# Optimization experiments

Measured on AMD Instinct MI355X. Metric: run time of the kernel, lower is better.

The kernel has to match this reference:

```python
import jax, jax.numpy as jnp
import numpy as np

B, NBANDS, NCHAN, NTIME = 32, 9, 64, 4096
M = 32
C = M * NBANDS          # 288 spectral-spatial channels
SF = 4                  # strideFactor
TLEN = 2 * SF - 1       # 7 overlapping temporal windows
E = 2                   # embed_dim
H = 2                   # num_heads (head_dim = 1)
NCLASS = 4
BN_EPS = 1e-5


def _renorm(w, maxnorm):
    # torch.renorm(p=2, dim=0): clamp L2 norm of each dim-0 slice to maxnorm
    norms = jnp.sqrt(jnp.sum(w.reshape(w.shape[0], -1) ** 2, axis=1))
    scale = jnp.minimum(1.0, maxnorm / jnp.maximum(norms, 1e-7))
    return w * scale.reshape((-1,) + (1,) * (w.ndim - 1))


def _pos_embed():
    # get_1d_sincos_pos_embed_from_grid(embed_dim=2, len=7)
    pos = np.arange(TLEN, dtype=np.float32)
    omega = 1.0 / (10000.0 ** (np.arange(E // 2, dtype=np.float32) / (E / 2.0)))
    out = pos[:, None] * omega[None, :]
    return jnp.asarray(np.concatenate([np.sin(out), np.cos(out)], axis=1), jnp.float32)  # [TLEN, E]


def setup_inputs() -> dict:
    key = jax.random.key(0)
    ks = jax.random.split(key, 10)
    s = 0.1
    return {
        "x": jax.random.uniform(ks[0], (B, NBANDS, NCHAN, NTIME), jnp.float32),
        "conv_w": jax.random.normal(ks[1], (C, 1, NCHAN, 1), jnp.float32) * s,
        "conv_b": jax.random.normal(ks[2], (C,), jnp.float32) * s,
        "bn_gamma": jnp.ones((C,), jnp.float32),
        "bn_beta": jnp.zeros((C,), jnp.float32),
        "bn_mean": jnp.zeros((C,), jnp.float32),
        "bn_var": jnp.ones((C,), jnp.float32),
        "in_proj_w": jax.random.normal(ks[3], (C, 3 * E, E), jnp.float32) * s,
        "in_proj_b": jax.random.normal(ks[4], (C, 3 * E), jnp.float32) * s,
        "out_proj_w": jax.random.normal(ks[5], (C, E, E), jnp.float32) * s,
        "out_proj_b": jax.random.normal(ks[6], (C, E), jnp.float32) * s,
        "last_w": jax.random.normal(ks[7], (NCLASS, C * TLEN * E), jnp.float32) * s,
        "last_b": jax.random.normal(ks[8], (NCLASS,), jnp.float32) * s,
    }


def _forward(x, conv_w, conv_b, bn_gamma, bn_beta, bn_mean, bn_var,
             in_proj_w, in_proj_b, out_proj_w, out_proj_b, last_w, last_b):
    # --- SCB: grouped conv (nChan,1) + BatchNorm(eval) + swish ---
    w = _renorm(conv_w, 2.0)
    y = jax.lax.conv_general_dilated(
        x, w, window_strides=(1, 1), padding='VALID',
        dimension_numbers=('NCHW', 'OIHW', 'NCHW'),
        feature_group_count=NBANDS) + conv_b[None, :, None, None]      # [B,C,1,NTIME]
    y = (y - bn_mean[None, :, None, None]) * jax.lax.rsqrt(bn_var + BN_EPS)[None, :, None, None]
    y = y * bn_gamma[None, :, None, None] + bn_beta[None, :, None, None]
    y = y * jax.nn.sigmoid(y)  # swish

    # --- overlapping temporal windows stacked on dim 2 ---
    ts = NTIME // (SF * 2)
    xs = jnp.concatenate([y[:, :, :, i * ts:(i + 2) * ts] for i in range(TLEN)], axis=2)  # [B,C,TLEN,2ts]

    # --- tempo_layer: log-var, RMS/mean shape factor ---
    var = jnp.log(jnp.clip(jnp.var(xs, axis=3, keepdims=True, ddof=1), 1e-6, 1e6))
    mean_ = jnp.mean(xs, axis=3, keepdims=True)
    x_rms = jnp.sqrt(jnp.mean(xs ** 2, axis=3, keepdims=True))
    feat = jnp.concatenate([var, x_rms / mean_], axis=3)               # [B,C,TLEN,E]

    # --- batched per-channel multihead self-attention (replaces C-way loop) ---
    yq = feat + _pos_embed()[None, None]                               # [B,C,T,E]
    qkv = jnp.einsum('bcte,cfe->bctf', yq, in_proj_w) + in_proj_b[None, :, None, :]
    q, k, v = jnp.split(qkv, 3, axis=3)
    hd = E // H
    q = q.reshape(B, C, TLEN, H, hd)
    k = k.reshape(B, C, TLEN, H, hd)
    v = v.reshape(B, C, TLEN, H, hd)
    scores = jnp.einsum('bcthd,bcshd->bchts', q, k) / jnp.sqrt(jnp.float32(hd))
    att = jax.nn.softmax(scores, axis=-1)
    o = jnp.einsum('bchts,bcshd->bcthd', att, v).reshape(B, C, TLEN, E)
    o = jnp.einsum('bcte,cfe->bctf', o, out_proj_w) + out_proj_b[None, :, None, :]

    # --- classifier with weight-norm constraint + log-softmax ---
    flat = o.reshape(B, C * TLEN * E)
    lw = _renorm(last_w, 0.5)
    logits = flat @ lw.T + last_b
    return jax.nn.log_softmax(logits, axis=1)


def reference(x, conv_w, conv_b, bn_gamma, bn_beta, bn_mean, bn_var,
              in_proj_w, in_proj_b, out_proj_w, out_proj_b, last_w, last_b):
    return _forward(x, conv_w, conv_b, bn_gamma, bn_beta, bn_mean, bn_var,
                    in_proj_w, in_proj_b, out_proj_w, out_proj_b, last_w, last_b)
```

## Files before the change

### kernel.cpp

```cpp
#include <hip/hip_runtime.h>
#include <math.h>

#define BB     32
#define NBANDS 9
#define NCHAN  64
#define NTIME  4096
#define CC     288
#define TLEN   7
#define NSEG   8
#define SEGLEN 512
#define NCLASS 4

#define WS_WF    0
#define WS_BIAS  (WS_WF + CC*NCHAN)
#define WS_S1    (WS_BIAS + CC)
#define WS_S2    (WS_S1 + BB*CC*NSEG)
#define WS_FLAT  (WS_S2 + BB*CC*NSEG)
#define WS_TOTAL (WS_FLAT + BB*CC*TLEN*2)

__global__ __launch_bounds__(64) void k0_fold(
    const float* __restrict__ cw, const float* __restrict__ cb,
    const float* __restrict__ gam, const float* __restrict__ bet,
    const float* __restrict__ mu, const float* __restrict__ var,
    float* __restrict__ Wf, float* __restrict__ biasf) {
  int c = blockIdx.x;
  int h = threadIdx.x;
  float w = cw[c * NCHAN + h];
  float sq = w * w;
#pragma unroll
  for (int off = 32; off; off >>= 1) sq += __shfl_down(sq, off, 64);
  sq = __shfl(sq, 0, 64);
  float norm = sqrtf(sq);
  float scale = fminf(1.0f, 2.0f / fmaxf(norm, 1e-7f));
  float bns = gam[c] / sqrtf(var[c] + 1e-5f);
  Wf[c * NCHAN + h] = w * scale * bns;
  if (h == 0) biasf[c] = (cb[c] - mu[c]) * bns + bet[c];
}

__global__ __launch_bounds__(256) void k1_conv(
    const float* __restrict__ x, const float* __restrict__ Wf,
    const float* __restrict__ biasf,
    float* __restrict__ S1, float* __restrict__ S2) {
  int gid = blockIdx.x;
  int seg = gid & 7;
  int g = (gid >> 3) % NBANDS;
  int b = gid / (NBANDS * NSEG);
  int tid = threadIdx.x;
  int tA = seg * SEGLEN + tid;
  int tB = tA + 256;
  const float* xp = x + (size_t)(b * NBANDS + g) * NCHAN * NTIME;

  float xa[NCHAN], xb[NCHAN];
#pragma unroll
  for (int h = 0; h < NCHAN; ++h) {
    xa[h] = xp[h * NTIME + tA];
    xb[h] = xp[h * NTIME + tB];
  }

  __shared__ float part[32][4][2];
  int wave = tid >> 6;
  int lane = tid & 63;
  const float* wbase = Wf + g * 32 * NCHAN;
  const float* bbase = biasf + g * 32;

  for (int c = 0; c < 32; ++c) {
    const float* wc = wbase + c * NCHAN;
    float bias = bbase[c];
    float da = bias, db = bias;
#pragma unroll
    for (int h = 0; h < NCHAN; ++h) {
      float w = wc[h];
      da = fmaf(w, xa[h], da);
      db = fmaf(w, xb[h], db);
    }
    float ya = da / (1.0f + __expf(-da));
    float yb = db / (1.0f + __expf(-db));
    float s1 = ya + yb;
    float s2 = ya * ya + yb * yb;
#pragma unroll
    for (int off = 32; off; off >>= 1) {
      s1 += __shfl_down(s1, off, 64);
      s2 += __shfl_down(s2, off, 64);
    }
    if (lane == 0) { part[c][wave][0] = s1; part[c][wave][1] = s2; }
  }
  __syncthreads();
  if (tid < 64) {
    int c = tid >> 1;
    int which = tid & 1;
    float v = part[c][0][which] + part[c][1][which] +
              part[c][2][which] + part[c][3][which];
    size_t o = (size_t)((b * CC) + g * 32 + c) * NSEG + seg;
    if (which == 0) S1[o] = v; else S2[o] = v;
  }
}

__global__ __launch_bounds__(256) void k2_attn(
    const float* __restrict__ S1, const float* __restrict__ S2,
    const float* __restrict__ ipw, const float* __restrict__ ipb,
    const float* __restrict__ opw, const float* __restrict__ opb,
    float* __restrict__ flat) {
  int idx = blockIdx.x * blockDim.x + threadIdx.x;
  if (idx >= BB * CC) return;
  int b = idx / CC, c = idx % CC;
  const float* s1 = S1 + (size_t)(b * CC + c) * NSEG;
  const float* s2 = S2 + (size_t)(b * CC + c) * NSEG;

  float yq[TLEN][2];
#pragma unroll
  for (int t = 0; t < TLEN; ++t) {
    float S1w = s1[t] + s1[t + 1];
    float S2w = s2[t] + s2[t + 1];
    float mean = S1w * (1.0f / 1024.0f);
    float var = (S2w - S1w * S1w * (1.0f / 1024.0f)) * (1.0f / 1023.0f);
    var = fminf(fmaxf(var, 1e-6f), 1e6f);
    float rms = sqrtf(S2w * (1.0f / 1024.0f));
    yq[t][0] = logf(var) + sinf((float)t);
    yq[t][1] = rms / mean + cosf((float)t);
  }

  const float* W = ipw + c * 12;
  const float* Bp = ipb + c * 6;
  float q[TLEN][2], k[TLEN][2], v[TLEN][2];
#pragma unroll
  for (int t = 0; t < TLEN; ++t) {
#pragma unroll
    for (int f = 0; f < 6; ++f) {
      float val = W[f * 2 + 0] * yq[t][0] + W[f * 2 + 1] * yq[t][1] + Bp[f];
      if (f < 2) q[t][f] = val;
      else if (f < 4) k[t][f - 2] = val;
      else v[t][f - 4] = val;
    }
  }

  float o[TLEN][2];
#pragma unroll
  for (int h = 0; h < 2; ++h) {
#pragma unroll
    for (int t = 0; t < TLEN; ++t) {
      float sc[TLEN];
      float m = -1e30f;
#pragma unroll
      for (int s = 0; s < TLEN; ++s) {
        sc[s] = q[t][h] * k[s][h];
        m = fmaxf(m, sc[s]);
      }
      float sum = 0.0f, acc = 0.0f;
#pragma unroll
      for (int s = 0; s < TLEN; ++s) {
        float e = expf(sc[s] - m);
        sum += e;
        acc += e * v[s][h];
      }
      o[t][h] = acc / sum;
    }
  }

  const float* Wo = opw + c * 4;
  const float* Bo = opb + c * 2;
  float* out = flat + (size_t)b * (CC * TLEN * 2) + c * (TLEN * 2);
#pragma unroll
  for (int t = 0; t < TLEN; ++t) {
    out[t * 2 + 0] = Wo[0] * o[t][0] + Wo[1] * o[t][1] + Bo[0];
    out[t * 2 + 1] = Wo[2] * o[t][0] + Wo[3] * o[t][1] + Bo[1];
  }
}

__global__ __launch_bounds__(256) void k3_cls(
    const float* __restrict__ flat, const float* __restrict__ lw,
    const float* __restrict__ lb, float* __restrict__ out) {
  const int FEAT = CC * TLEN * 2;
  int b = blockIdx.x;
  int tid = threadIdx.x;
  const float* f = flat + (size_t)b * FEAT;
  float d[NCLASS] = {0, 0, 0, 0}, n2[NCLASS] = {0, 0, 0, 0};
  for (int j = tid; j < FEAT; j += 256) {
    float fv = f[j];
#pragma unroll
    for (int n = 0; n < NCLASS; ++n) {
      float w = lw[n * FEAT + j];
      d[n] = fmaf(fv, w, d[n]);
      n2[n] = fmaf(w, w, n2[n]);
    }
  }
  __shared__ float red[4][8];
  int lane = tid & 63, wave = tid >> 6;
#pragma unroll
  for (int n = 0; n < NCLASS; ++n) {
#pragma unroll
    for (int off = 32; off; off >>= 1) {
      d[n] += __shfl_down(d[n], off, 64);
      n2[n] += __shfl_down(n2[n], off, 64);
    }
  }
  if (lane == 0) {
#pragma unroll
    for (int n = 0; n < NCLASS; ++n) {
      red[wave][n] = d[n];
      red[wave][n + 4] = n2[n];
    }
  }
  __syncthreads();
  if (tid == 0) {
    float logit[NCLASS];
#pragma unroll
    for (int n = 0; n < NCLASS; ++n) {
      float dn = red[0][n] + red[1][n] + red[2][n] + red[3][n];
      float nn = red[0][n + 4] + red[1][n + 4] + red[2][n + 4] + red[3][n + 4];
      float norm = sqrtf(nn);
      float scale = fminf(1.0f, 0.5f / fmaxf(norm, 1e-7f));
      logit[n] = dn * scale + lb[n];
    }
    float m = fmaxf(fmaxf(logit[0], logit[1]), fmaxf(logit[2], logit[3]));
    float s = 0.0f;
#pragma unroll
    for (int n = 0; n < NCLASS; ++n) s += expf(logit[n] - m);
    float ls = logf(s);
#pragma unroll
    for (int n = 0; n < NCLASS; ++n) out[b * NCLASS + n] = logit[n] - m - ls;
  }
}

extern "C" void kernel_launch(void* const* d_in, const int* in_sizes, int n_in,
                              void* d_out, int out_size, void* d_ws, size_t ws_size,
                              hipStream_t stream) {
  const float* x     = (const float*)d_in[0];
  const float* cw    = (const float*)d_in[1];
  const float* cb    = (const float*)d_in[2];
  const float* gam   = (const float*)d_in[3];
  const float* bet   = (const float*)d_in[4];
  const float* mu    = (const float*)d_in[5];
  const float* var   = (const float*)d_in[6];
  const float* ipw   = (const float*)d_in[7];
  const float* ipb   = (const float*)d_in[8];
  const float* opw   = (const float*)d_in[9];
  const float* opb   = (const float*)d_in[10];
  const float* lw    = (const float*)d_in[11];
  const float* lb    = (const float*)d_in[12];
  float* out = (float*)d_out;

  float* ws = (float*)d_ws;
  float* Wf    = ws + WS_WF;
  float* biasf = ws + WS_BIAS;
  float* S1    = ws + WS_S1;
  float* S2    = ws + WS_S2;
  float* flat  = ws + WS_FLAT;

  k0_fold<<<CC, 64, 0, stream>>>(cw, cb, gam, bet, mu, var, Wf, biasf);
  k1_conv<<<BB * NBANDS * NSEG, 256, 0, stream>>>(x, Wf, biasf, S1, S2);
  k2_attn<<<(BB * CC + 255) / 256, 256, 0, stream>>>(S1, S2, ipw, ipb, opw, opb, flat);
  k3_cls<<<BB, 256, 0, stream>>>(flat, lw, lb, out);
}
```

Baseline: 504.9 us.

## Restructure conv kernel to stream channel tiles with register accumulators

The grouped-conv kernel no longer preloads all 64 input channels for two timesteps into registers. It now loops over channel tiles of 8, loads float2-vectorized inputs per tile, and keeps 64 accumulators for the 32 output channels, with launch bounds raised to 4 blocks per CU. This is meant to cut register pressure and improve load coalescing and occupancy. The attention kernel also gets constant sin/cos tables and fast log/exp/rcp intrinsics, at a small cost in accuracy.

Measured after the change: 455.6 us. 1.11x faster.

```diff
diff --git a/kernel.cpp b/kernel.cpp
--- a/kernel.cpp
+++ b/kernel.cpp
@@ -37,7 +37,7 @@
   if (h == 0) biasf[c] = (cb[c] - mu[c]) * bns + bet[c];
 }
 
-__global__ __launch_bounds__(256) void k1_conv(
+__global__ __launch_bounds__(256, 4) void k1_conv(
     const float* __restrict__ x, const float* __restrict__ Wf,
     const float* __restrict__ biasf,
     float* __restrict__ S1, float* __restrict__ S2) {
@@ -46,37 +46,44 @@
   int g = (gid >> 3) % NBANDS;
   int b = gid / (NBANDS * NSEG);
   int tid = threadIdx.x;
-  int tA = seg * SEGLEN + tid;
-  int tB = tA + 256;
-  const float* xp = x + (size_t)(b * NBANDS + g) * NCHAN * NTIME;
-
-  float xa[NCHAN], xb[NCHAN];
-#pragma unroll
-  for (int h = 0; h < NCHAN; ++h) {
-    xa[h] = xp[h * NTIME + tA];
-    xb[h] = xp[h * NTIME + tB];
+  const float* xp = x + (size_t)(b * NBANDS + g) * NCHAN * NTIME + seg * SEGLEN;
+  const float* wbase = Wf + g * 32 * NCHAN;
+  const float* bbase = biasf + g * 32;
+
+  float acc0[32], acc1[32];
+#pragma unroll
+  for (int c = 0; c < 32; ++c) { acc0[c] = 0.0f; acc1[c] = 0.0f; }
+
+#pragma unroll 1
+  for (int ht = 0; ht < NCHAN; ht += 8) {
+    float2 xv[8];
+#pragma unroll
+    for (int j = 0; j < 8; ++j)
+      xv[j] = ((const float2*)(xp + (size_t)(ht + j) * NTIME))[tid];
+#pragma unroll
+    for (int c = 0; c < 32; ++c) {
+#pragma unroll
+      for (int j = 0; j < 8; ++j) {
+        float w = wbase[c * NCHAN + ht + j];
+        acc0[c] = fmaf(w, xv[j].x, acc0[c]);
+        acc1[c] = fmaf(w, xv[j].y, acc1[c]);
+      }
+    }
   }
 
   __shared__ float part[32][4][2];
   int wave = tid >> 6;
   int lane = tid & 63;
-  const float* wbase = Wf + g * 32 * NCHAN;
-  const float* bbase = biasf + g * 32;
-
+
+#pragma unroll
   for (int c = 0; c < 32; ++c) {
-    const float* wc = wbase + c * NCHAN;
     float bias = bbase[c];
-    float da = bias, db = bias;
-#pragma unroll
-    for (int h = 0; h < NCHAN; ++h) {
-      float w = wc[h];
-      da = fmaf(w, xa[h], da);
-      db = fmaf(w, xb[h], db);
-    }
-    float ya = da / (1.0f + __expf(-da));
-    float yb = db / (1.0f + __expf(-db));
+    float da = acc0[c] + bias;
+    float db = acc1[c] + bias;
+    float ya = da * __builtin_amdgcn_rcpf(1.0f + __expf(-da));
+    float yb = db * __builtin_amdgcn_rcpf(1.0f + __expf(-db));
     float s1 = ya + yb;
-    float s2 = ya * ya + yb * yb;
+    float s2 = fmaf(ya, ya, yb * yb);
 #pragma unroll
     for (int off = 32; off; off >>= 1) {
       s1 += __shfl_down(s1, off, 64);
@@ -100,6 +107,10 @@
     const float* __restrict__ ipw, const float* __restrict__ ipb,
     const float* __restrict__ opw, const float* __restrict__ opb,
     float* __restrict__ flat) {
+  const float PSIN[TLEN] = {0.0f, 0.8414709848f, 0.9092974268f, 0.1411200081f,
+                            -0.7568024953f, -0.9589242747f, -0.2794154982f};
+  const float PCOS[TLEN] = {1.0f, 0.5403023059f, -0.4161468365f, -0.9899924966f,
+                            -0.6536436209f, 0.2836621855f, 0.9601702867f};
   int idx = blockIdx.x * blockDim.x + threadIdx.x;
   if (idx >= BB * CC) return;
   int b = idx / CC, c = idx % CC;
@@ -115,8 +126,8 @@
     float var = (S2w - S1w * S1w * (1.0f / 1024.0f)) * (1.0f / 1023.0f);
     var = fminf(fmaxf(var, 1e-6f), 1e6f);
     float rms = sqrtf(S2w * (1.0f / 1024.0f));
-    yq[t][0] = logf(var) + sinf((float)t);
-    yq[t][1] = rms / mean + cosf((float)t);
+    yq[t][0] = __logf(var) + PSIN[t];
+    yq[t][1] = rms / mean + PCOS[t];
   }
 
   const float* W = ipw + c * 12;
@@ -148,7 +159,7 @@
       float sum = 0.0f, acc = 0.0f;
 #pragma unroll
       for (int s = 0; s < TLEN; ++s) {
-        float e = expf(sc[s] - m);
+        float e = __expf(sc[s] - m);
         sum += e;
         acc += e * v[s][h];
       }
```
